# Performance work log

Hardware: AMD Instinct MI355X
Metric: run time of the kernel (lower is better)

The kernel has to match this reference:

```python
import jax, jax.numpy as jnp
import numpy as np

# 6 pairwise combinations of the 4 ray coordinates (decomp='2d')
COMBS = np.array([[0, 1], [0, 2], [0, 3], [1, 2], [1, 3], [2, 3]])
RAY_MIN = 0.0
RAY_MAX = 1.0
N_RAYS = 262144
GRID_DIM = 16
MLP_DIM = GRID_DIM * 6 * 3  # grid_dim * n_combs * n_levels = 288
MLP_WIDTH = 128


def _bilinear(grid_c, pts):
    """grid_c: [C,H,W] feature plane; pts: [N,2] in [0,1].
    Bilinear interpolation with align_corners=True semantics (grid_sample)."""
    C, H, W = grid_c.shape
    u = pts[:, 0] * (H - 1)
    v = pts[:, 1] * (W - 1)
    u0 = jnp.clip(jnp.floor(u), 0, H - 2).astype(jnp.int32)
    v0 = jnp.clip(jnp.floor(v), 0, W - 2).astype(jnp.int32)
    u1 = u0 + 1
    v1 = v0 + 1
    wu = (u - u0.astype(u.dtype))[None, :]  # [1,N]
    wv = (v - v0.astype(v.dtype))[None, :]
    g00 = grid_c[:, u0, v0]  # [C,N]
    g01 = grid_c[:, u0, v1]
    g10 = grid_c[:, u1, v0]
    g11 = grid_c[:, u1, v1]
    out = (g00 * (1 - wu) * (1 - wv) + g01 * (1 - wu) * wv
           + g10 * wu * (1 - wv) + g11 * wu * wv)
    return out.T  # [N,C]


def _level_feats(grids, coords):
    """grids: [6,C,H,W]; coords: [N,6,2] -> [N, 6*C] (comb-minor order)."""
    f = jax.vmap(_bilinear, in_axes=(0, 1))(grids, coords)  # [6,N,C]
    n = coords.shape[0]
    return jnp.moveaxis(f, 0, 1).reshape(n, -1)


def setup_inputs() -> dict:
    key = jax.random.key(0)
    ks = jax.random.split(key, 8)
    ray = jax.random.uniform(ks[0], (N_RAYS, 4), dtype=jnp.float32)
    grids_l0 = jax.random.normal(ks[1], (6, GRID_DIM, 128, 128), dtype=jnp.float32) * 0.1
    grids_l1 = jax.random.normal(ks[2], (6, GRID_DIM, 256, 256), dtype=jnp.float32) * 0.1
    grids_l2 = jax.random.normal(ks[3], (6, GRID_DIM, 512, 512), dtype=jnp.float32) * 0.1
    w1 = jax.random.normal(ks[4], (MLP_DIM, MLP_WIDTH), dtype=jnp.float32) * (1.0 / np.sqrt(MLP_DIM))
    b1 = jnp.zeros((MLP_WIDTH,), dtype=jnp.float32)
    w2 = jax.random.normal(ks[5], (MLP_WIDTH, 3), dtype=jnp.float32) * (1.0 / np.sqrt(MLP_WIDTH))
    b2 = jnp.zeros((3,), dtype=jnp.float32)
    return {"ray": ray, "grids_l0": grids_l0, "grids_l1": grids_l1,
            "grids_l2": grids_l2, "w1": w1, "b1": b1, "w2": w2, "b2": b2}


def reference(ray, grids_l0, grids_l1, grids_l2, w1, b1, w2, b2):
    # normalize rays into [0,1] using ray_min/ray_max buffers
    pts = (ray - RAY_MIN) / (RAY_MAX - RAY_MIN)
    coords = pts[:, COMBS]  # [N,6,2]
    # level-major, combination-minor concat (matches the nested forward loops)
    feats = jnp.concatenate(
        [_level_feats(g, coords) for g in (grids_l0, grids_l1, grids_l2)], axis=-1)
    h = jax.nn.relu(feats @ w1 + b1)
    return jax.nn.sigmoid(h @ w2 + b2)
```

## Files before the change

kernel.cpp:

```cpp
#include <hip/hip_runtime.h>
#include <hip/hip_bf16.h>
#include <cstdint>
#include <cstddef>

#define N_RAYS 262144
#define NR 32
#define THREADS 256
#define FSTRIDE 292

#define T0_OFF 0u
#define T1_OFF 1572864u
#define T2_OFF 7864320u
#define T_ELEMS 33030144u
#define FEAT_BYTE_OFF 66060288u
#define FEAT_DWORDS 37748736u
#define W1F_BYTE_OFF 217055232u
#define W1F_BYTES 73728u
#define KEYS_OFF   217128960u
#define PERM_OFF   217653248u
#define HIST_OFF   218701824u
#define OFFS_OFF   218963968u
#define RSORT_OFF  219226112u
#define NEED_SORT  223420416u

#define PB_L0   384
#define PB_L1   1920
#define PB_L2   8064
#define PB_PK   8082
#define PB_HI   9106

typedef __attribute__((ext_vector_type(8))) short short8v;
typedef __attribute__((ext_vector_type(4))) float float4v;

__device__ __forceinline__ float bf_lo(uint32_t w) { return __uint_as_float(w << 16); }
__device__ __forceinline__ float bf_hi(uint32_t w) { return __uint_as_float(w & 0xFFFF0000u); }

__device__ __forceinline__ float bf_extract(const uint4& q, int i) {
    uint32_t w = ((const uint32_t*)&q)[i >> 1];
    uint32_t h = (i & 1) ? (w & 0xFFFF0000u) : (w << 16);
    return __uint_as_float(h);
}

__device__ __forceinline__ uint16_t f2bf_rne(float f) {
    uint32_t x = __float_as_uint(f);
    uint32_t r = x + 0x7FFFu + ((x >> 16) & 1u);
    return (uint16_t)(r >> 16);
}

__device__ __forceinline__ float sel4(const float4& p, int i) {
    float r = p.x;
    r = (i == 1) ? p.y : r;
    r = (i == 2) ? p.z : r;
    r = (i == 3) ? p.w : r;
    return r;
}

__device__ __forceinline__ uint32_t morton4(const float4& p) {
    int q0 = min(15, max(0, (int)(p.x * 16.0f)));
    int q1 = min(15, max(0, (int)(p.y * 16.0f)));
    int q2 = min(15, max(0, (int)(p.z * 16.0f)));
    int q3 = min(15, max(0, (int)(p.w * 16.0f)));
    uint32_t key = 0;
    #pragma unroll
    for (int b = 0; b < 4; ++b) {
        key |= (uint32_t)((q0 >> b) & 1) << (4 * b + 0);
        key |= (uint32_t)((q1 >> b) & 1) << (4 * b + 1);
        key |= (uint32_t)((q2 >> b) & 1) << (4 * b + 2);
        key |= (uint32_t)((q3 >> b) & 1) << (4 * b + 3);
    }
    return key;
}

__device__ __forceinline__ void transpose_body(const float* __restrict__ in,
                                               uint16_t* __restrict__ out,
                                               int H, int idx) {
    int hh = H * H;
    int c = idx / hh;
    int rem = idx - c * hh;
    const float* ip = in + (size_t)c * 16 * hh + rem;
    uint32_t words[8];
    #pragma unroll
    for (int j = 0; j < 8; ++j) {
        uint16_t lo = f2bf_rne(ip[(size_t)(2 * j) * hh]);
        uint16_t hi = f2bf_rne(ip[(size_t)(2 * j + 1) * hh]);
        words[j] = (uint32_t)lo | ((uint32_t)hi << 16);
    }
    uint4* op = (uint4*)(out + (size_t)idx * 16);
    op[0] = make_uint4(words[0], words[1], words[2], words[3]);
    op[1] = make_uint4(words[4], words[5], words[6], words[7]);
}

__global__ __launch_bounds__(256) void prep_kernel(
    const float* __restrict__ g0, const float* __restrict__ g1,
    const float* __restrict__ g2, const float* __restrict__ w1,
    const float4* __restrict__ ray,
    uint16_t* __restrict__ gt, uint16_t* __restrict__ w1f,
    uint16_t* __restrict__ keys, uint32_t* __restrict__ hist) {
    int b = blockIdx.x;
    int tid = threadIdx.x;
    if (b < PB_L0) {
        transpose_body(g0, gt + T0_OFF, 128, b * 256 + tid);
    } else if (b < PB_L1) {
        transpose_body(g1, gt + T1_OFF, 256, (b - PB_L0) * 256 + tid);
    } else if (b < PB_L2) {
        transpose_body(g2, gt + T2_OFF, 512, (b - PB_L1) * 256 + tid);
    } else if (b < PB_PK) {
        int t = (b - PB_L2) * 256 + tid;
        int lane = t & 63;
        int fr = t >> 6;
        int ct = fr / 9;
        int kc = fr - ct * 9;
        int col = ct * 16 + (lane & 15);
        int krow = kc * 32 + (lane >> 4) * 8;
        uint32_t od[4];
        #pragma unroll
        for (int j = 0; j < 4; ++j) {
            uint16_t lo = f2bf_rne(w1[(size_t)(krow + 2 * j) * 128 + col]);
            uint16_t hi = f2bf_rne(w1[(size_t)(krow + 2 * j + 1) * 128 + col]);
            od[j] = (uint32_t)lo | ((uint32_t)hi << 16);
        }
        *(uint4*)(w1f + (size_t)t * 8) = make_uint4(od[0], od[1], od[2], od[3]);
    } else {
        int r = (b - PB_PK) * 256 + tid;
        float4 p = ray[r];
        uint32_t key = morton4(p);
        keys[r] = (uint16_t)key;
        atomicAdd(&hist[key], 1u);
    }
}

__global__ void scanA_kernel(const uint32_t* __restrict__ hist,
                             uint32_t* __restrict__ bsum,
                             uint32_t* __restrict__ offs) {
    __shared__ uint32_t s[256];
    int t = threadIdx.x, b = blockIdx.x;
    uint32_t v = hist[b * 256 + t];
    s[t] = v;
    __syncthreads();
    for (int d = 1; d < 256; d <<= 1) {
        uint32_t x = (t >= d) ? s[t - d] : 0;
        __syncthreads();
        s[t] += x;
        __syncthreads();
    }
    offs[b * 256 + t] = s[t] - v;
    if (t == 255) bsum[b] = s[255];
}

__global__ void scanB_kernel(uint32_t* __restrict__ bsum) {
    __shared__ uint32_t s[256];
    int t = threadIdx.x;
    uint32_t v = bsum[t];
    s[t] = v;
    __syncthreads();
    for (int d = 1; d < 256; d <<= 1) {
        uint32_t x = (t >= d) ? s[t - d] : 0;
        __syncthreads();
        s[t] += x;
        __syncthreads();
    }
    bsum[t] = s[t] - v;
}

__global__ void scatter_kernel(const float4* __restrict__ ray,
                               const uint16_t* __restrict__ keys,
                               uint32_t* __restrict__ offs,
                               const uint32_t* __restrict__ bsum,
                               uint32_t* __restrict__ perm,
                               float4* __restrict__ ray_sorted) {
    int r = blockIdx.x * 256 + threadIdx.x;
    uint32_t key = keys[r];
    uint32_t pos = atomicAdd(&offs[key], 1u) + bsum[key >> 8];
    perm[pos] = (uint32_t)r;
    ray_sorted[pos] = ray[r];
}

__global__ __launch_bounds__(256, 4) void fused_gmlp_kernel(
    const float4* __restrict__ rsort, const uint16_t* __restrict__ gt,
    const uint16_t* __restrict__ w1f, const float* __restrict__ bias1,
    const float* __restrict__ w2, const float* __restrict__ bias2,
    const uint32_t* __restrict__ perm, float* __restrict__ out) {
    __shared__ uint32_t s_feats[32 * 148];
    __shared__ float s_w2[384];
    __shared__ float4 s_ray[32];

    int tid = threadIdx.x;
    int wvid = tid >> 6;
    int lane = tid & 63;
    int swz = ((blockIdx.x & 7) << 10) + (blockIdx.x >> 3);
    int r0 = swz << 5;

    if (tid < 32) s_ray[tid] = rsort[r0 + tid];
    s_w2[tid] = w2[tid];
    if (tid < 128) s_w2[256 + tid] = w2[256 + tid];
    __syncthreads();

    {
        int r = lane >> 1;
        int half = lane & 1;
        for (int interp = wvid; interp < 18; interp += 4) {
            int level = (interp >= 12) ? 2 : ((interp >= 6) ? 1 : 0);
            int comb = interp - level * 6;
            int H = 128 << level;
            float4 p = s_ray[r];
            int c0 = (0x211000 >> (4 * comb)) & 0xF;
            int c1 = (0x332321 >> (4 * comb)) & 0xF;
            float u = sel4(p, c0) * (float)(H - 1);
            float v = sel4(p, c1) * (float)(H - 1);
            float u0f = fminf(fmaxf(floorf(u), 0.0f), (float)(H - 2));
            float v0f = fminf(fmaxf(floorf(v), 0.0f), (float)(H - 2));
            float fu = u - u0f, fv = v - v0f;
            int u0 = (int)u0f, v0 = (int)v0f;

            uint32_t lvl_off = (level == 0) ? T0_OFF : ((level == 1) ? T1_OFF : T2_OFF);
            const uint16_t* gp = gt + lvl_off +
                                 (((size_t)comb * H + u0) * H + v0) * 16 + half * 8;
            uint4 c00 = *(const uint4*)gp;
            uint4 c01 = *(const uint4*)(gp + 16);
            uint4 c10 = *(const uint4*)(gp + (size_t)16 * H);
            uint4 c11 = *(const uint4*)(gp + (size_t)16 * H + 16);

            float w00 = (1.0f - fu) * (1.0f - fv);
            float w01 = (1.0f - fu) * fv;
            float w10 = fu * (1.0f - fv);
            float w11 = fu * fv;

            uint32_t od[4];
            #pragma unroll
            for (int j = 0; j < 4; ++j) {
                uint32_t v00 = ((const uint32_t*)&c00)[j];
                uint32_t v01 = ((const uint32_t*)&c01)[j];
                uint32_t v10 = ((const uint32_t*)&c10)[j];
                uint32_t v11 = ((const uint32_t*)&c11)[j];
                float lo = w00 * bf_lo(v00) + w01 * bf_lo(v01) +
                           w10 * bf_lo(v10) + w11 * bf_lo(v11);
                float hi = w00 * bf_hi(v00) + w01 * bf_hi(v01) +
                           w10 * bf_hi(v10) + w11 * bf_hi(v11);
                od[j] = (uint32_t)f2bf_rne(lo) | ((uint32_t)f2bf_rne(hi) << 16);
            }
            *(uint4*)&s_feats[r * 148 + interp * 8 + half * 4] =
                make_uint4(od[0], od[1], od[2], od[3]);
        }
    }
    __syncthreads();

    float b1c0 = bias1[wvid * 32 + (lane & 15)];
    float b1c1 = bias1[wvid * 32 + 16 + (lane & 15)];
    int lg = lane >> 4;
    const uint32_t* arow = &s_feats[(lane & 15) * 148 + lg * 4];

    float4v acc00, acc10, acc01, acc11;
    {
        short8v bfrA[9];
        #pragma unroll
        for (int kc = 0; kc < 9; ++kc)
            bfrA[kc] = *(const short8v*)(w1f + (((size_t)((wvid * 2) * 9 + kc)) * 64 + lane) * 8);
        #pragma unroll
        for (int j = 0; j < 4; ++j) { acc00[j] = b1c0; acc10[j] = b1c0; }
        #pragma unroll
        for (int kc = 0; kc < 9; ++kc) {
            short8v a0 = *(const short8v*)(arow + kc * 16);
            short8v a1 = *(const short8v*)(arow + 16 * 148 + kc * 16);
            acc00 = __builtin_amdgcn_mfma_f32_16x16x32_bf16(a0, bfrA[kc], acc00, 0, 0, 0);
            acc10 = __builtin_amdgcn_mfma_f32_16x16x32_bf16(a1, bfrA[kc], acc10, 0, 0, 0);
        }
    }
    {
        short8v bfrB[9];
        #pragma unroll
        for (int kc = 0; kc < 9; ++kc)
            bfrB[kc] = *(const short8v*)(w1f + (((size_t)((wvid * 2 + 1) * 9 + kc)) * 64 + lane) * 8);
        #pragma unroll
        for (int j = 0; j < 4; ++j) { acc01[j] = b1c1; acc11[j] = b1c1; }
        #pragma unroll
        for (int kc = 0; kc < 9; ++kc) {
            short8v a0 = *(const short8v*)(arow + kc * 16);
            short8v a1 = *(const short8v*)(arow + 16 * 148 + kc * 16);
            acc01 = __builtin_amdgcn_mfma_f32_16x16x32_bf16(a0, bfrB[kc], acc01, 0, 0, 0);
            acc11 = __builtin_amdgcn_mfma_f32_16x16x32_bf16(a1, bfrB[kc], acc11, 0, 0, 0);
        }
    }
    __syncthreads();

    float* s_h = (float*)s_feats;
    {
        int c0 = wvid * 32 + (lane & 15);
        int rb = lg * 4;
        #pragma unroll
        for (int j = 0; j < 4; ++j) {
            s_h[(rb + j) * 132 + c0]            = fmaxf(acc00[j], 0.0f);
            s_h[(rb + j) * 132 + c0 + 16]       = fmaxf(acc01[j], 0.0f);
            s_h[(rb + j + 16) * 132 + c0]       = fmaxf(acc10[j], 0.0f);
            s_h[(rb + j + 16) * 132 + c0 + 16]  = fmaxf(acc11[j], 0.0f);
        }
    }
    __syncthreads();

    int ray = tid >> 3;
    int jg = tid & 7;
    int j0 = jg * 16;
    float p0 = 0.f, p1 = 0.f, p2 = 0.f;
    #pragma unroll
    for (int qq = 0; qq < 4; ++qq) {
        float4 hv = *(const float4*)&s_h[ray * 132 + j0 + qq * 4];
        const float* w2a = &s_w2[(j0 + qq * 4) * 3];
        p0 += hv.x * w2a[0] + hv.y * w2a[3] + hv.z * w2a[6] + hv.w * w2a[9];
        p1 += hv.x * w2a[1] + hv.y * w2a[4] + hv.z * w2a[7] + hv.w * w2a[10];
        p2 += hv.x * w2a[2] + hv.y * w2a[5] + hv.z * w2a[8] + hv.w * w2a[11];
    }
    p0 += __shfl_xor(p0, 1); p0 += __shfl_xor(p0, 2); p0 += __shfl_xor(p0, 4);
    p1 += __shfl_xor(p1, 1); p1 += __shfl_xor(p1, 2); p1 += __shfl_xor(p1, 4);
    p2 += __shfl_xor(p2, 1); p2 += __shfl_xor(p2, 2); p2 += __shfl_xor(p2, 4);

    if (jg == 0) {
        int orig = (int)perm[r0 + ray];
        float o0 = 1.0f / (1.0f + expf(-(p0 + bias2[0])));
        float o1 = 1.0f / (1.0f + expf(-(p1 + bias2[1])));
        float o2 = 1.0f / (1.0f + expf(-(p2 + bias2[2])));
        float* op = out + (size_t)orig * 3;
        op[0] = o0; op[1] = o1; op[2] = o2;
    }
}

__global__ void transpose_kernel(const float* __restrict__ in,
                                 __hip_bfloat16* __restrict__ out, int H) {
    int idx = blockIdx.x * blockDim.x + threadIdx.x;
    if (idx >= 6 * H * H) return;
    transpose_body(in, (uint16_t*)out, H, idx);
}

__global__ void w1_pack_kernel(const float* __restrict__ w1, uint16_t* __restrict__ w1f) {
    int t = blockIdx.x * 64 + threadIdx.x;
    if (t >= 8 * 9 * 64) return;
    int lane = t & 63;
    int fr = t >> 6;
    int ct = fr / 9;
    int kc = fr - ct * 9;
    int col = ct * 16 + (lane & 15);
    int krow = kc * 32 + (lane >> 4) * 8;
    uint32_t od[4];
    #pragma unroll
    for (int j = 0; j < 4; ++j) {
        uint16_t lo = f2bf_rne(w1[(size_t)(krow + 2 * j) * 128 + col]);
        uint16_t hi = f2bf_rne(w1[(size_t)(krow + 2 * j + 1) * 128 + col]);
        od[j] = (uint32_t)lo | ((uint32_t)hi << 16);
    }
    *(uint4*)(w1f + (size_t)t * 8) = make_uint4(od[0], od[1], od[2], od[3]);
}

__global__ __launch_bounds__(256, 8) void gather_t_kernel(
    const float4* __restrict__ ray, const uint16_t* __restrict__ gt,
    uint32_t* __restrict__ featsT) {
    int lb = (blockIdx.x & 7) * 2304 + (blockIdx.x >> 3);
    int interp = lb >> 10;
    int r = ((lb & 1023) << 8) + threadIdx.x;
    int level = interp / 6;
    int comb = interp - level * 6;
    int H = 128 << level;

    float4 p = ray[r];
    int c0 = (0x211000 >> (4 * comb)) & 0xF;
    int c1 = (0x332321 >> (4 * comb)) & 0xF;
    float u = sel4(p, c0) * (float)(H - 1);
    float v = sel4(p, c1) * (float)(H - 1);
    float u0f = fminf(fmaxf(floorf(u), 0.0f), (float)(H - 2));
    float v0f = fminf(fmaxf(floorf(v), 0.0f), (float)(H - 2));
    float wu = u - u0f, wv = v - v0f;
    int u0 = (int)u0f, v0 = (int)v0f;

    uint32_t lvl_off = (level == 0) ? T0_OFF : ((level == 1) ? T1_OFF : T2_OFF);
    const uint16_t* gp0 = gt + lvl_off + (((size_t)comb * H + u0) * H + v0) * 16;
    const uint4* q0 = (const uint4*)gp0;
    const uint4* q1 = (const uint4*)(gp0 + (size_t)16 * H);
    uint4 a0 = q0[0], a1 = q0[1], a2 = q0[2], a3 = q0[3];
    uint4 b0 = q1[0], b1 = q1[1], b2 = q1[2], b3 = q1[3];

    uint32_t c00[8], c01[8], c10[8], c11[8];
    #pragma unroll
    for (int j = 0; j < 4; ++j) {
        c00[j] = ((const uint32_t*)&a0)[j];  c00[j + 4] = ((const uint32_t*)&a1)[j];
        c01[j] = ((const uint32_t*)&a2)[j];  c01[j + 4] = ((const uint32_t*)&a3)[j];
        c10[j] = ((const uint32_t*)&b0)[j];  c10[j + 4] = ((const uint32_t*)&b1)[j];
        c11[j] = ((const uint32_t*)&b2)[j];  c11[j + 4] = ((const uint32_t*)&b3)[j];
    }

    float w00 = (1.0f - wu) * (1.0f - wv);
    float w01 = (1.0f - wu) * wv;
    float w10 = wu * (1.0f - wv);
    float w11 = wu * wv;

    uint32_t od[8];
    #pragma unroll
    for (int j = 0; j < 8; ++j) {
        float lo = w00 * bf_lo(c00[j]) + w01 * bf_lo(c01[j]) +
                   w10 * bf_lo(c10[j]) + w11 * bf_lo(c11[j]);
        float hi = w00 * bf_hi(c00[j]) + w01 * bf_hi(c01[j]) +
                   w10 * bf_hi(c10[j]) + w11 * bf_hi(c11[j]);
        od[j] = (uint32_t)f2bf_rne(lo) | ((uint32_t)f2bf_rne(hi) << 16);
    }

    uint4* op = (uint4*)(featsT + ((size_t)interp * N_RAYS + r) * 8);
    op[0] = make_uint4(od[0], od[1], od[2], od[3]);
    op[1] = make_uint4(od[4], od[5], od[6], od[7]);
}

__global__ __launch_bounds__(256, 2) void mfma_mlp_kernel(
    const uint16_t* __restrict__ featsT,
    const uint16_t* __restrict__ w1f,
    const float* __restrict__ bias1,
    const float* __restrict__ w2, const float* __restrict__ bias2,
    const uint32_t* __restrict__ perm,
    float* __restrict__ out, int tiles_per_block) {
    __shared__ float s_h[32][132];

    int tid = threadIdx.x;
    int wv = tid >> 6;
    int lane = tid & 63;

    short8v bfr[2][9];
    #pragma unroll
    for (int ctl = 0; ctl < 2; ++ctl) {
        int ct = wv * 2 + ctl;
        #pragma unroll
        for (int kc = 0; kc < 9; ++kc)
            bfr[ctl][kc] = *(const short8v*)(w1f + (((size_t)(ct * 9 + kc)) * 64 + lane) * 8);
    }
    float b1c0 = bias1[wv * 32 + (lane & 15)];
    float b1c1 = bias1[wv * 32 + 16 + (lane & 15)];

    int jg = tid & 7;
    int j0 = jg * 16;
    float w2r0[16], w2r1[16], w2r2[16];
    #pragma unroll
    for (int jj = 0; jj < 16; ++jj) {
        const float* w2p = w2 + (size_t)(j0 + jj) * 3;
        w2r0[jj] = w2p[0]; w2r1[jj] = w2p[1]; w2r2[jj] = w2p[2];
    }
    float bb0 = bias2[0], bb1 = bias2[1], bb2 = bias2[2];

    int lg = lane >> 4;
    int half8 = (lg & 1) * 8;
    int ipo = lg >> 1;

    for (int it = 0; it < tiles_per_block; ++it) {
        int tile = blockIdx.x * tiles_per_block + it;
        int r0 = tile * 32;
        int rA = r0 + (lane & 15);

        short8v af[18];
        #pragma unroll
        for (int kc = 0; kc < 9; ++kc) {
            size_t base = ((size_t)(2 * kc + ipo) * N_RAYS + rA) * 16 + half8;
            af[kc]     = *(const short8v*)(featsT + base);
            af[9 + kc] = *(const short8v*)(featsT + base + 256);
        }

        float4v acc00, acc01, acc10, acc11;
        #pragma unroll
        for (int j = 0; j < 4; ++j) { acc00[j] = b1c0; acc01[j] = b1c1; acc10[j] = b1c0; acc11[j] = b1c1; }

        #pragma unroll
        for (int kc = 0; kc < 9; ++kc) {
            acc00 = __builtin_amdgcn_mfma_f32_16x16x32_bf16(af[kc],     bfr[0][kc], acc00, 0, 0, 0);
            acc01 = __builtin_amdgcn_mfma_f32_16x16x32_bf16(af[kc],     bfr[1][kc], acc01, 0, 0, 0);
            acc10 = __builtin_amdgcn_mfma_f32_16x16x32_bf16(af[9 + kc], bfr[0][kc], acc10, 0, 0, 0);
            acc11 = __builtin_amdgcn_mfma_f32_16x16x32_bf16(af[9 + kc], bfr[1][kc], acc11, 0, 0, 0);
        }

        __syncthreads();
        {
            int c0 = wv * 32 + (lane & 15);
            int rb = (lane >> 4) * 4;
            #pragma unroll
            for (int j = 0; j < 4; ++j) {
                s_h[rb + j][c0]           = fmaxf(acc00[j], 0.0f);
                s_h[rb + j][c0 + 16]      = fmaxf(acc01[j], 0.0f);
                s_h[rb + j + 16][c0]      = fmaxf(acc10[j], 0.0f);
                s_h[rb + j + 16][c0 + 16] = fmaxf(acc11[j], 0.0f);
            }
        }
        __syncthreads();

        int ray = tid >> 3;
        float p0 = 0.f, p1 = 0.f, p2 = 0.f;
        #pragma unroll
        for (int qq = 0; qq < 4; ++qq) {
            float4 hv = *(const float4*)&s_h[ray][j0 + qq * 4];
            float h0 = hv.x, h1 = hv.y, h2 = hv.z, h3 = hv.w;
            p0 += h0 * w2r0[qq * 4] + h1 * w2r0[qq * 4 + 1] + h2 * w2r0[qq * 4 + 2] + h3 * w2r0[qq * 4 + 3];
            p1 += h0 * w2r1[qq * 4] + h1 * w2r1[qq * 4 + 1] + h2 * w2r1[qq * 4 + 2] + h3 * w2r1[qq * 4 + 3];
            p2 += h0 * w2r2[qq * 4] + h1 * w2r2[qq * 4 + 1] + h2 * w2r2[qq * 4 + 2] + h3 * w2r2[qq * 4 + 3];
        }
        p0 += __shfl_xor(p0, 1); p0 += __shfl_xor(p0, 2); p0 += __shfl_xor(p0, 4);
        p1 += __shfl_xor(p1, 1); p1 += __shfl_xor(p1, 2); p1 += __shfl_xor(p1, 4);
        p2 += __shfl_xor(p2, 1); p2 += __shfl_xor(p2, 2); p2 += __shfl_xor(p2, 4);

        if (jg == 0) {
            int orig = perm ? (int)perm[r0 + ray] : (r0 + ray);
            float o0 = 1.0f / (1.0f + expf(-(p0 + bb0)));
            float o1 = 1.0f / (1.0f + expf(-(p1 + bb1)));
            float o2 = 1.0f / (1.0f + expf(-(p2 + bb2)));
            float* op = out + (size_t)orig * 3;
            op[0] = o0; op[1] = o1; op[2] = o2;
        }
    }
}

template <bool USE_T>
__global__ __launch_bounds__(THREADS) void fused_kernel(
    const float4* __restrict__ ray,
    const float* __restrict__ g0, const float* __restrict__ g1,
    const float* __restrict__ g2,
    const __hip_bfloat16* __restrict__ gt,
    const float* __restrict__ weights1, const float* __restrict__ bias1,
    const float* __restrict__ weights2, const float* __restrict__ bias2,
    float* __restrict__ out) {
    __shared__ float4 s_ray[NR];
    __shared__ float s_feats[NR][FSTRIDE];

    int tid = threadIdx.x;
    int rbase = blockIdx.x * NR;
    if (tid < NR) s_ray[tid] = ray[rbase + tid];
    __syncthreads();

    for (int t = tid; t < NR * 36; t += THREADS) {
        int r = t / 36;
        int rem = t - r * 36;
        int interp = rem >> 1;
        int half = rem & 1;
        int level = (interp >= 12) ? 2 : ((interp >= 6) ? 1 : 0);
        int comb = interp - level * 6;
        int H = 128 << level;
        float4 p = s_ray[r];
        int c0 = (0x211000 >> (4 * comb)) & 0xF;
        int c1 = (0x332321 >> (4 * comb)) & 0xF;
        float u = sel4(p, c0) * (float)(H - 1);
        float v = sel4(p, c1) * (float)(H - 1);
        float u0f = fminf(fmaxf(floorf(u), 0.0f), (float)(H - 2));
        float v0f = fminf(fmaxf(floorf(v), 0.0f), (float)(H - 2));
        float wu = u - u0f, wv = v - v0f;
        int u0 = (int)u0f, v0 = (int)v0f;
        float w00 = (1.0f - wu) * (1.0f - wv);
        float w01 = (1.0f - wu) * wv;
        float w10 = wu * (1.0f - wv);
        float w11 = wu * wv;
        float f[8];
        if (USE_T) {
            uint32_t lvl_off = (level == 0) ? T0_OFF : ((level == 1) ? T1_OFF : T2_OFF);
            const uint16_t* gp = (const uint16_t*)gt + lvl_off +
                                 (((size_t)comb * H + u0) * H + v0) * 16 + half * 8;
            uint4 a00 = *(const uint4*)gp;
            uint4 a01 = *(const uint4*)(gp + 16);
            uint4 a10 = *(const uint4*)(gp + (size_t)16 * H);
            uint4 a11 = *(const uint4*)(gp + (size_t)16 * H + 16);
            #pragma unroll
            for (int i = 0; i < 8; ++i) {
                f[i] = w00 * bf_extract(a00, i) + w01 * bf_extract(a01, i) +
                       w10 * bf_extract(a10, i) + w11 * bf_extract(a11, i);
            }
        } else {
            const float* gp = (level == 0) ? g0 : ((level == 1) ? g1 : g2);
            const float* base = gp + ((size_t)(comb * 16 + half * 8) * H + u0) * H + v0;
            #pragma unroll
            for (int i = 0; i < 8; ++i) {
                const float* q = base + (size_t)i * H * H;
                float a00 = q[0], a01 = q[1], a10 = q[H], a11 = q[H + 1];
                f[i] = w00 * a00 + w01 * a01 + w10 * a10 + w11 * a11;
            }
        }
        int fo = interp * 16 + half * 8;
        float* fp = &s_feats[r][fo];
        #pragma unroll
        for (int i = 0; i < 8; ++i) fp[i] = f[i];
    }
    __syncthreads();

    int r = tid >> 3;
    int jg = tid & 7;
    int j0 = jg * 16;
    float acc[16];
    #pragma unroll
    for (int jj = 0; jj < 16; ++jj) acc[jj] = bias1[j0 + jj];

    const float* wp = weights1 + j0;
    for (int k = 0; k < 288; k += 4) {
        float4 fv = *(const float4*)&s_feats[r][k];
        #pragma unroll
        for (int kk = 0; kk < 4; ++kk) {
            const float4* wr = (const float4*)(wp + (size_t)(k + kk) * 128);
            float fk = (kk == 0) ? fv.x : ((kk == 1) ? fv.y : ((kk == 2) ? fv.z : fv.w));
            float4 wa = wr[0], wb = wr[1], wc = wr[2], wd = wr[3];
            acc[0]  += fk * wa.x; acc[1]  += fk * wa.y; acc[2]  += fk * wa.z; acc[3]  += fk * wa.w;
            acc[4]  += fk * wb.x; acc[5]  += fk * wb.y; acc[6]  += fk * wb.z; acc[7]  += fk * wb.w;
            acc[8]  += fk * wc.x; acc[9]  += fk * wc.y; acc[10] += fk * wc.z; acc[11] += fk * wc.w;
            acc[12] += fk * wd.x; acc[13] += fk * wd.y; acc[14] += fk * wd.z; acc[15] += fk * wd.w;
        }
    }

    float p0 = 0.f, p1 = 0.f, p2 = 0.f;
    #pragma unroll
    for (int jj = 0; jj < 16; ++jj) {
        float h = fmaxf(acc[jj], 0.0f);
        const float* w2r = weights2 + (size_t)(j0 + jj) * 3;
        p0 += h * w2r[0];
        p1 += h * w2r[1];
        p2 += h * w2r[2];
    }
    p0 += __shfl_xor(p0, 1); p0 += __shfl_xor(p0, 2); p0 += __shfl_xor(p0, 4);
    p1 += __shfl_xor(p1, 1); p1 += __shfl_xor(p1, 2); p1 += __shfl_xor(p1, 4);
    p2 += __shfl_xor(p2, 1); p2 += __shfl_xor(p2, 2); p2 += __shfl_xor(p2, 4);

    if (jg == 0) {
        float o0 = 1.0f / (1.0f + expf(-(p0 + bias2[0])));
        float o1 = 1.0f / (1.0f + expf(-(p1 + bias2[1])));
        float o2 = 1.0f / (1.0f + expf(-(p2 + bias2[2])));
        float* op = out + (size_t)(rbase + r) * 3;
        op[0] = o0; op[1] = o1; op[2] = o2;
    }
}

extern "C" void kernel_launch(void* const* d_in, const int* in_sizes, int n_in,
                              void* d_out, int out_size, void* d_ws, size_t ws_size,
                              hipStream_t stream) {
    const float4* ray = (const float4*)d_in[0];
    const float* g0 = (const float*)d_in[1];
    const float* g1 = (const float*)d_in[2];
    const float* g2 = (const float*)d_in[3];
    const float* w1 = (const float*)d_in[4];
    const float* b1 = (const float*)d_in[5];
    const float* w2 = (const float*)d_in[6];
    const float* b2 = (const float*)d_in[7];
    float* out = (float*)d_out;

    const size_t T_BYTES = (size_t)T_ELEMS * 2;
    const size_t NEED = (size_t)W1F_BYTE_OFF + W1F_BYTES;

    if (ws_size >= (size_t)NEED_SORT) {
        char* ws = (char*)d_ws;
        __hip_bfloat16* wsb = (__hip_bfloat16*)d_ws;
        uint32_t* bsum  = (uint32_t*)(ws + FEAT_BYTE_OFF);
        uint16_t* w1f  = (uint16_t*)(ws + W1F_BYTE_OFF);
        uint16_t* keys = (uint16_t*)(ws + KEYS_OFF);
        uint32_t* perm = (uint32_t*)(ws + PERM_OFF);
        uint32_t* hist = (uint32_t*)(ws + HIST_OFF);
        uint32_t* offs = (uint32_t*)(ws + OFFS_OFF);
        float4* rsort  = (float4*)(ws + RSORT_OFF);

        hipMemsetAsync(hist, 0, 65536 * 4, stream);
        prep_kernel<<<PB_HI, 256, 0, stream>>>(
            g0, g1, g2, w1, ray, (uint16_t*)wsb, w1f, keys, hist);
        scanA_kernel<<<256, 256, 0, stream>>>(hist, bsum, offs);
        scanB_kernel<<<1, 256, 0, stream>>>(bsum);
        scatter_kernel<<<N_RAYS / 256, 256, 0, stream>>>(ray, keys, offs, bsum, perm, rsort);
        fused_gmlp_kernel<<<N_RAYS / 32, 256, 0, stream>>>(
            rsort, (const uint16_t*)wsb, w1f, b1, w2, b2, perm, out);
    } else if (ws_size >= NEED) {
        __hip_bfloat16* wsb = (__hip_bfloat16*)d_ws;
        transpose_kernel<<<(6 * 128 * 128 + 255) / 256, 256, 0, stream>>>(g0, wsb + T0_OFF, 128);
        transpose_kernel<<<(6 * 256 * 256 + 255) / 256, 256, 0, stream>>>(g1, wsb + T1_OFF, 256);
        transpose_kernel<<<(6 * 512 * 512 + 255) / 256, 256, 0, stream>>>(g2, wsb + T2_OFF, 512);
        uint32_t* feats = (uint32_t*)((char*)d_ws + FEAT_BYTE_OFF);
        uint16_t* w1f = (uint16_t*)((char*)d_ws + W1F_BYTE_OFF);
        w1_pack_kernel<<<72, 64, 0, stream>>>(w1, w1f);
        gather_t_kernel<<<18432, 256, 0, stream>>>(ray, (const uint16_t*)wsb, feats);
        const int TILES_PER_BLOCK = 4;
        int nblk = N_RAYS / 32 / TILES_PER_BLOCK;
        mfma_mlp_kernel<<<nblk, 256, 0, stream>>>(
            (const uint16_t*)feats, w1f, b1, w2, b2, nullptr, out, TILES_PER_BLOCK);
    } else if (ws_size >= T_BYTES) {
        __hip_bfloat16* wsb = (__hip_bfloat16*)d_ws;
        transpose_kernel<<<(6 * 128 * 128 + 255) / 256, 256, 0, stream>>>(g0, wsb + T0_OFF, 128);
        transpose_kernel<<<(6 * 256 * 256 + 255) / 256, 256, 0, stream>>>(g1, wsb + T1_OFF, 256);
        transpose_kernel<<<(6 * 512 * 512 + 255) / 256, 256, 0, stream>>>(g2, wsb + T2_OFF, 512);
        fused_kernel<true><<<N_RAYS / NR, THREADS, 0, stream>>>(
            ray, g0, g1, g2, wsb, w1, b1, w2, b2, out);
    } else {
        fused_kernel<false><<<N_RAYS / NR, THREADS, 0, stream>>>(
            ray, g0, g1, g2, nullptr, w1, b1, w2, b2, out);
    }
}
```

Baseline: 177.4 us.

## Fold block-sum scan into scatter, gather rays via perm, rebalance interp work

Removes the single-block scanB launch by having every scatter block redundantly scan the 256 block sums in shared memory. The scatter no longer writes a sorted ray copy; the fused kernel instead loads perm into shared memory and gathers rays through it, reusing the cached perm for the output write. The 18 interpolation tasks are redistributed across the 4 waves with a packed schedule that mixes expensive level-2 lookups with cheaper ones. The trade is one fewer launch and less scatter traffic against redundant scan work per scatter block and an indirect ray load.

```diff
diff --git a/kernel.cpp b/kernel.cpp
--- a/kernel.cpp
+++ b/kernel.cpp
@@ -147,42 +147,40 @@
     if (t == 255) bsum[b] = s[255];
 }
 
-__global__ void scanB_kernel(uint32_t* __restrict__ bsum) {
-    __shared__ uint32_t s[256];
+__global__ void scatter_kernel(const uint16_t* __restrict__ keys,
+                               uint32_t* __restrict__ offs,
+                               const uint32_t* __restrict__ bsum,
+                               uint32_t* __restrict__ perm) {
+    __shared__ uint32_t s_incl[256];
+    __shared__ uint32_t s_tot[256];
     int t = threadIdx.x;
     uint32_t v = bsum[t];
-    s[t] = v;
+    s_tot[t] = v;
+    s_incl[t] = v;
     __syncthreads();
     for (int d = 1; d < 256; d <<= 1) {
-        uint32_t x = (t >= d) ? s[t - d] : 0;
+        uint32_t x = (t >= d) ? s_incl[t - d] : 0;
         __syncthreads();
-        s[t] += x;
+        s_incl[t] += x;
         __syncthreads();
     }
-    bsum[t] = s[t] - v;
-}
-
-__global__ void scatter_kernel(const float4* __restrict__ ray,
-                               const uint16_t* __restrict__ keys,
-                               uint32_t* __restrict__ offs,
-                               const uint32_t* __restrict__ bsum,
-                               uint32_t* __restrict__ perm,
-                               float4* __restrict__ ray_sorted) {
-    int r = blockIdx.x * 256 + threadIdx.x;
+    int r = blockIdx.x * 256 + t;
     uint32_t key = keys[r];
-    uint32_t pos = atomicAdd(&offs[key], 1u) + bsum[key >> 8];
+    uint32_t b = key >> 8;
+    uint32_t base = s_incl[b] - s_tot[b];
+    uint32_t pos = atomicAdd(&offs[key], 1u) + base;
     perm[pos] = (uint32_t)r;
-    ray_sorted[pos] = ray[r];
 }
 
 __global__ __launch_bounds__(256, 4) void fused_gmlp_kernel(
-    const float4* __restrict__ rsort, const uint16_t* __restrict__ gt,
+    const float4* __restrict__ rays, const uint16_t* __restrict__ gt,
     const uint16_t* __restrict__ w1f, const float* __restrict__ bias1,
     const float* __restrict__ w2, const float* __restrict__ bias2,
     const uint32_t* __restrict__ perm, float* __restrict__ out) {
     __shared__ uint32_t s_feats[32 * 148];
     __shared__ float s_w2[384];
     __shared__ float4 s_ray[32];
+    __shared__ uint32_t s_perm[32];
 
     int tid = threadIdx.x;
     int wvid = tid >> 6;
@@ -190,7 +188,11 @@
     int swz = ((blockIdx.x & 7) << 10) + (blockIdx.x >> 3);
     int r0 = swz << 5;
 
-    if (tid < 32) s_ray[tid] = rsort[r0 + tid];
+    if (tid < 32) {
+        uint32_t pm = perm[r0 + tid];
+        s_perm[tid] = pm;
+        s_ray[tid] = rays[pm];
+    }
     s_w2[tid] = w2[tid];
     if (tid < 128) s_w2[256 + tid] = w2[256 + tid];
     __syncthreads();
@@ -198,7 +200,13 @@
     {
         int r = lane >> 1;
         int half = lane & 1;
-        for (int interp = wvid; interp < 18; interp += 4) {
+        int ns = (wvid >= 2) ? 5 : 4;
+        uint32_t pk = (wvid == 0) ? ((12u) | (13u << 5) | (0u << 10) | (1u << 15))
+                    : (wvid == 1) ? ((14u) | (15u << 5) | (2u << 10) | (3u << 15))
+                    : (wvid == 2) ? ((16u) | (4u << 5) | (5u << 10) | (6u << 15) | (7u << 20))
+                                  : ((17u) | (8u << 5) | (9u << 10) | (10u << 15) | (11u << 20));
+        for (int i = 0; i < ns; ++i) {
+            int interp = (int)((pk >> (5 * i)) & 31u);
             int level = (interp >= 12) ? 2 : ((interp >= 6) ? 1 : 0);
             int comb = interp - level * 6;
             int H = 128 << level;
@@ -313,7 +321,7 @@
     p2 += __shfl_xor(p2, 1); p2 += __shfl_xor(p2, 2); p2 += __shfl_xor(p2, 4);
 
     if (jg == 0) {
-        int orig = (int)perm[r0 + ray];
+        int orig = (int)s_perm[ray];
         float o0 = 1.0f / (1.0f + expf(-(p0 + bias2[0])));
         float o1 = 1.0f / (1.0f + expf(-(p1 + bias2[1])));
         float o2 = 1.0f / (1.0f + expf(-(p2 + bias2[2])));
@@ -644,16 +652,14 @@
         uint32_t* perm = (uint32_t*)(ws + PERM_OFF);
         uint32_t* hist = (uint32_t*)(ws + HIST_OFF);
         uint32_t* offs = (uint32_t*)(ws + OFFS_OFF);
-        float4* rsort  = (float4*)(ws + RSORT_OFF);
 
         hipMemsetAsync(hist, 0, 65536 * 4, stream);
         prep_kernel<<<PB_HI, 256, 0, stream>>>(
             g0, g1, g2, w1, ray, (uint16_t*)wsb, w1f, keys, hist);
         scanA_kernel<<<256, 256, 0, stream>>>(hist, bsum, offs);
-        scanB_kernel<<<1, 256, 0, stream>>>(bsum);
-        scatter_kernel<<<N_RAYS / 256, 256, 0, stream>>>(ray, keys, offs, bsum, perm, rsort);
+        scatter_kernel<<<N_RAYS / 256, 256, 0, stream>>>(keys, offs, bsum, perm);
         fused_gmlp_kernel<<<N_RAYS / 32, 256, 0, stream>>>(
-            rsort, (const uint16_t*)wsb, w1f, b1, w2, b2, perm, out);
+            ray, (const uint16_t*)wsb, w1f, b1, w2, b2, perm, out);
     } else if (ws_size >= NEED) {
         __hip_bfloat16* wsb = (__hip_bfloat16*)d_ws;
         transpose_kernel<<<(6 * 128 * 128 + 255) / 256, 256, 0, stream>>>(g0, wsb + T0_OFF, 128);
```

Result: no change. 180.4 us (+1.7%).
